# Kernel optimization log

Measured on AMD Instinct MI355X. Metric: run time of the kernel, lower is better.

The kernel has to match this reference:

```python
import jax, jax.numpy as jnp
import numpy as np

N = 20000      # nodes
E = 640000     # edges (avg degree 32)
F_IN = 128     # node_features
H = 128        # hidden_channels
OUT = 64       # output_features


def setup_inputs() -> dict:
    key = jax.random.key(0)
    ks = jax.random.split(key, 12)
    s = 0.05
    return {
        "x": jax.random.normal(ks[0], (N, F_IN), jnp.float32),
        "edge_index": jax.random.randint(ks[1], (2, E), 0, N, dtype=jnp.int64),
        "W1": jax.random.normal(ks[2], (F_IN, H), jnp.float32) * s,
        "b1": jnp.zeros((H,), jnp.float32),
        "W2": jax.random.normal(ks[3], (H, H), jnp.float32) * s,
        "b2": jnp.zeros((H,), jnp.float32),
        "W_ih": jax.random.normal(ks[4], (4 * H, H), jnp.float32) * s,
        "W_hh": jax.random.normal(ks[5], (4 * H, H), jnp.float32) * s,
        "b_ih": jnp.zeros((4 * H,), jnp.float32),
        "b_hh": jnp.zeros((4 * H,), jnp.float32),
        "W_lin": jax.random.normal(ks[6], (OUT, H), jnp.float32) * s,
        "b_lin": jnp.zeros((OUT,), jnp.float32),
    }


def gcn_conv(x, edge_index, W, b):
    # PyG GCNConv: add self-loops, symmetric normalization D^-1/2 A D^-1/2
    n = x.shape[0]
    loop = jnp.arange(n, dtype=edge_index.dtype)
    src = jnp.concatenate([edge_index[0], loop])
    dst = jnp.concatenate([edge_index[1], loop])
    deg = jax.ops.segment_sum(jnp.ones(src.shape[0], x.dtype), dst, num_segments=n)
    dinv = jnp.where(deg > 0, jax.lax.rsqrt(deg), 0.0)
    norm = dinv[src] * dinv[dst]                 # [E+N]
    xw = x @ W                                   # [N, H] transform before aggregate
    msg = xw[src] * norm[:, None]                # gather + scale
    out = jax.ops.segment_sum(msg, dst, num_segments=n)  # scatter-add
    return out + b


def lstm_seq(xs, W_ih, W_hh, b_ih, b_hh):
    # single-layer LSTM over sequence xs: [T, H_in], batch of 1 (squeezed).
    h_dim = W_hh.shape[1]
    h0 = jnp.zeros((h_dim,), xs.dtype)

    def step(carry, xt):
        h, c = carry
        g = xt @ W_ih.T + b_ih + h @ W_hh.T + b_hh
        i, f, gg, o = jnp.split(g, 4)
        i = jax.nn.sigmoid(i)
        f = jax.nn.sigmoid(f)
        gg = jnp.tanh(gg)
        o = jax.nn.sigmoid(o)
        c = f * c + i * gg
        h = o * jnp.tanh(c)
        return (h, c), h

    _, hs = jax.lax.scan(step, (h0, h0), xs)
    return hs  # [T, H]


def reference(x, edge_index, W1, b1, W2, b2, W_ih, W_hh, b_ih, b_hh, W_lin, b_lin):
    h = jax.nn.relu(gcn_conv(x, edge_index, W1, b1))
    # dropout(p=0.2) is identity in eval mode
    h = jax.nn.relu(gcn_conv(h, edge_index, W2, b2))
    hs = lstm_seq(h, W_ih, W_hh, b_ih, b_hh)     # nodes treated as one sequence
    return hs @ W_lin.T + b_lin                  # [N, OUT]
```

## Files before the change

kernel.cpp:

```cpp
#include <hip/hip_runtime.h>
#include <cstdint>

#define NF 128
#define G4 512

typedef float v2f __attribute__((ext_vector_type(2)));

__device__ __forceinline__ float frcp(float x) { return __builtin_amdgcn_rcpf(x); }
__device__ __forceinline__ float ftanh(float x) {
  float e = __expf(2.f * x);
  return 1.f - 2.f * frcp(e + 1.f);
}

__device__ __forceinline__ float dpp_xor1(float x) {
  int r = __builtin_amdgcn_update_dpp(0, __float_as_int(x), 0xB1, 0xF, 0xF, true);
  return __int_as_float(r);
}
__device__ __forceinline__ float dpp_xor2(float x) {
  int r = __builtin_amdgcn_update_dpp(0, __float_as_int(x), 0x4E, 0xF, 0xF, true);
  return __int_as_float(r);
}


__global__ void k_fill(float* p, float v, int n) {
  int i = blockIdx.x * blockDim.x + threadIdx.x;
  if (i < n) p[i] = v;
}

__global__ void k_detect_i64(const int* e, int npairs, int* flag) {
  int f = 1;
  for (int i = 1; i < 2 * npairs; i += 2)
    if (e[i] != 0) { f = 0; break; }
  *flag = f;
}

__device__ __forceinline__ int eidx(const void* edges, int i64, size_t pos) {
  if (i64) return (int)((const long long*)edges)[pos];
  return ((const int*)edges)[pos];
}

__global__ void k_count(const void* __restrict__ edges, const int* __restrict__ flag,
                        float* __restrict__ deg, int E) {
  int e = blockIdx.x * blockDim.x + threadIdx.x;
  if (e < E) {
    int d = eidx(edges, *flag, (size_t)E + e);
    unsafeAtomicAdd(&deg[d], 1.0f);
  }
}

__global__ void k_rsqrt(float* p, int n) {
  int i = blockIdx.x * blockDim.x + threadIdx.x;
  if (i < n) p[i] = rsqrtf(p[i]);
}

__global__ void k_t128(const float* __restrict__ in, float* __restrict__ out) {
  int n = blockIdx.x, k = threadIdx.x;
  out[n * 128 + k] = in[k * 128 + n];
}

__global__ void k_add(const float* a, const float* b, float* o, int n) {
  int i = blockIdx.x * blockDim.x + threadIdx.x;
  if (i < n) o[i] = a[i] + b[i];
}

__global__ void k_wprep(const float* __restrict__ W, float* __restrict__ wp) {
  int t = blockIdx.x;
  int j = threadIdx.x;
  int u = t >> 2, p = t & 3;
  int g = j >> 5, k = j & 31;
  wp[(size_t)t * 128 + j] = W[(size_t)(g * 128 + u) * 128 + 32 * p + k];
}

__global__ __launch_bounds__(256)
void gemm_bt(const float* __restrict__ A, const float* __restrict__ B,
             const float* __restrict__ bias, float* __restrict__ C,
             int M, int N, int K) {
  __shared__ float As[32][68];
  __shared__ float Bs[32][68];
  const int bm = blockIdx.x * 64;
  const int bn = blockIdx.y * 64;
  const int tid = threadIdx.x;
  const int tm = (tid & 15) << 2;
  const int tn = (tid >> 4) << 2;
  float acc[4][4] = {};

  for (int k0 = 0; k0 < K; k0 += 32) {
#pragma unroll
    for (int l = 0; l < 2; ++l) {
      int idx = tid + l * 256;
      int row = idx >> 3;
      int k4 = (idx & 7) << 2;
      int ar = bm + row; ar = ar < M ? ar : M - 1;
      float4 av = *(const float4*)(A + (size_t)ar * K + k0 + k4);
      As[k4 + 0][row] = av.x; As[k4 + 1][row] = av.y;
      As[k4 + 2][row] = av.z; As[k4 + 3][row] = av.w;
      int br = bn + row; br = br < N ? br : N - 1;
      float4 bv = *(const float4*)(B + (size_t)br * K + k0 + k4);
      Bs[k4 + 0][row] = bv.x; Bs[k4 + 1][row] = bv.y;
      Bs[k4 + 2][row] = bv.z; Bs[k4 + 3][row] = bv.w;
    }
    __syncthreads();
#pragma unroll
    for (int kk = 0; kk < 32; ++kk) {
      float4 a = *(const float4*)&As[kk][tm];
      float4 b = *(const float4*)&Bs[kk][tn];
      float av[4] = {a.x, a.y, a.z, a.w};
      float bv[4] = {b.x, b.y, b.z, b.w};
#pragma unroll
      for (int i = 0; i < 4; ++i)
#pragma unroll
        for (int jj = 0; jj < 4; ++jj)
          acc[i][jj] = __builtin_fmaf(av[i], bv[jj], acc[i][jj]);
    }
    __syncthreads();
  }

  float4 bv4;
  if (bias) bv4 = *(const float4*)(bias + bn + tn);
  else bv4 = make_float4(0.f, 0.f, 0.f, 0.f);
#pragma unroll
  for (int i = 0; i < 4; ++i) {
    int row = bm + tm + i;
    if (row < M) {
      float4 v;
      v.x = acc[i][0] + bv4.x;
      v.y = acc[i][1] + bv4.y;
      v.z = acc[i][2] + bv4.z;
      v.w = acc[i][3] + bv4.w;
      *(float4*)(C + (size_t)row * N + bn + tn) = v;
    }
  }
}

__global__ __launch_bounds__(256)
void k_aggregate(const float* __restrict__ xw, const void* __restrict__ edges,
                 const int* __restrict__ flag, const float* __restrict__ dinv,
                 float* __restrict__ out, int E) {
  int e = blockIdx.x * 8 + (threadIdx.x >> 5);
  if (e >= E) return;
  int i64 = *flag;
  int s = eidx(edges, i64, e);
  int d = eidx(edges, i64, (size_t)E + e);
  float nrm = dinv[s] * dinv[d];
  int f4 = threadIdx.x & 31;
  float4 v = ((const float4*)xw)[(size_t)s * 32 + f4];
  float* op = out + (size_t)d * 128 + f4 * 4;
  unsafeAtomicAdd(op + 0, v.x * nrm);
  unsafeAtomicAdd(op + 1, v.y * nrm);
  unsafeAtomicAdd(op + 2, v.z * nrm);
  unsafeAtomicAdd(op + 3, v.w * nrm);
}

__global__ void k_finish(float* __restrict__ h, const float* __restrict__ xw,
                         const float* __restrict__ dinv, const float* __restrict__ b,
                         int N) {
  int i4 = blockIdx.x * blockDim.x + threadIdx.x;
  if (i4 >= N * 32) return;
  int n = i4 >> 5;
  int f4 = (i4 & 31) << 2;
  float di = dinv[n];
  float s = di * di;
  float4 ag = ((const float4*)h)[i4];
  float4 xv = ((const float4*)xw)[i4];
  float4 bv = *(const float4*)(b + f4);
  float4 r;
  r.x = fmaxf(__builtin_fmaf(xv.x, s, ag.x) + bv.x, 0.f);
  r.y = fmaxf(__builtin_fmaf(xv.y, s, ag.y) + bv.y, 0.f);
  r.z = fmaxf(__builtin_fmaf(xv.z, s, ag.z) + bv.z, 0.f);
  r.w = fmaxf(__builtin_fmaf(xv.w, s, ag.w) + bv.w, 0.f);
  ((float4*)h)[i4] = r;
}

__global__ __launch_bounds__(512)
__attribute__((amdgpu_waves_per_eu(2, 2)))
void k_lstm(const float* __restrict__ g_in, const float* __restrict__ wp,
            float* __restrict__ hs, int T) {
  const int t = threadIdx.x;
  const int q = t >> 2;
  const int pos = t & 3;
  const int row = pos * 128 + q;

  __shared__ __align__(16) float hbuf[2][144];
  __shared__ float lds_cap[20736];

  if (t == 0) {
    volatile float* vp = lds_cap;
    vp[0] = 0.f;
  }

  {
    const float* wr = wp + (size_t)t * 128;
    asm volatile(
      "global_load_dwordx4 v[128:131], %0, off\n\t"
      "global_load_dwordx4 v[132:135], %0, off offset:16\n\t"
      "global_load_dwordx4 v[136:139], %0, off offset:32\n\t"
      "global_load_dwordx4 v[140:143], %0, off offset:48\n\t"
      "global_load_dwordx4 v[144:147], %0, off offset:64\n\t"
      "global_load_dwordx4 v[148:151], %0, off offset:80\n\t"
      "global_load_dwordx4 v[152:155], %0, off offset:96\n\t"
      "global_load_dwordx4 v[156:159], %0, off offset:112\n\t"
      "global_load_dwordx4 v[160:163], %0, off offset:128\n\t"
      "global_load_dwordx4 v[164:167], %0, off offset:144\n\t"
      "global_load_dwordx4 v[168:171], %0, off offset:160\n\t"
      "global_load_dwordx4 v[172:175], %0, off offset:176\n\t"
      "global_load_dwordx4 v[176:179], %0, off offset:192\n\t"
      "global_load_dwordx4 v[180:183], %0, off offset:208\n\t"
      "global_load_dwordx4 v[184:187], %0, off offset:224\n\t"
      "global_load_dwordx4 v[188:191], %0, off offset:240\n\t"
      "global_load_dwordx4 v[192:195], %0, off offset:256\n\t"
      "global_load_dwordx4 v[196:199], %0, off offset:272\n\t"
      "global_load_dwordx4 v[200:203], %0, off offset:288\n\t"
      "global_load_dwordx4 v[204:207], %0, off offset:304\n\t"
      "global_load_dwordx4 v[208:211], %0, off offset:320\n\t"
      "global_load_dwordx4 v[212:215], %0, off offset:336\n\t"
      "global_load_dwordx4 v[216:219], %0, off offset:352\n\t"
      "global_load_dwordx4 v[220:223], %0, off offset:368\n\t"
      "global_load_dwordx4 v[224:227], %0, off offset:384\n\t"
      "global_load_dwordx4 v[228:231], %0, off offset:400\n\t"
      "global_load_dwordx4 v[232:235], %0, off offset:416\n\t"
      "global_load_dwordx4 v[236:239], %0, off offset:432\n\t"
      "global_load_dwordx4 v[240:243], %0, off offset:448\n\t"
      "global_load_dwordx4 v[244:247], %0, off offset:464\n\t"
      "global_load_dwordx4 v[248:251], %0, off offset:480\n\t"
      "global_load_dwordx4 v[252:255], %0, off offset:496\n\t"
      "s_waitcnt vmcnt(0)"
      :: "v"(wr)
      : "v128","v129","v130","v131","v132","v133","v134","v135",
        "v136","v137","v138","v139","v140","v141","v142","v143",
        "v144","v145","v146","v147","v148","v149","v150","v151",
        "v152","v153","v154","v155","v156","v157","v158","v159",
        "v160","v161","v162","v163","v164","v165","v166","v167",
        "v168","v169","v170","v171","v172","v173","v174","v175",
        "v176","v177","v178","v179","v180","v181","v182","v183",
        "v184","v185","v186","v187","v188","v189","v190","v191",
        "v192","v193","v194","v195","v196","v197","v198","v199",
        "v200","v201","v202","v203","v204","v205","v206","v207",
        "v208","v209","v210","v211","v212","v213","v214","v215",
        "v216","v217","v218","v219","v220","v221","v222","v223",
        "v224","v225","v226","v227","v228","v229","v230","v231",
        "v232","v233","v234","v235","v236","v237","v238","v239",
        "v240","v241","v242","v243","v244","v245","v246","v247",
        "v248","v249","v250","v251","v252","v253","v254","v255");
  }

  if (t < 144) { hbuf[0][t] = 0.f; hbuf[1][t] = 0.f; }
  float c = 0.f;
  float gn = g_in[row];

  const uint32_t adr0 = (uint32_t)(uintptr_t)&hbuf[0][36 * pos];
  const uint32_t adr1 = (uint32_t)(uintptr_t)&hbuf[1][36 * pos];

  __syncthreads();

  int pb = 0;
  const bool isg = (pos == 2);
  const bool sw1 = (pos & 1);
  const bool sw2 = (pos & 2) != 0;

  for (int step = 0; step < T; ++step) {
    float gcur = gn;
    size_t nb = (size_t)(step + 1 < T ? step + 1 : step) * G4;
    gn = g_in[nb + row];

    uint32_t adr = pb ? adr1 : adr0;
    v2f a0, a1, a2, a3;
    asm volatile(
      "ds_read_b128 v[96:99], %4\n\t"
      "ds_read_b128 v[100:103], %4 offset:16\n\t"
      "ds_read_b128 v[104:107], %4 offset:32\n\t"
      "ds_read_b128 v[108:111], %4 offset:48\n\t"
      "ds_read_b128 v[112:115], %4 offset:64\n\t"
      "ds_read_b128 v[116:119], %4 offset:80\n\t"
      "ds_read_b128 v[120:123], %4 offset:96\n\t"
      "ds_read_b128 v[124:127], %4 offset:112\n\t"
      "s_waitcnt lgkmcnt(0)\n\t"
      "v_pk_mul_f32 %0, v[128:129], v[96:97]\n\t"
      "v_pk_mul_f32 %1, v[160:161], v[96:97]\n\t"
      "v_pk_mul_f32 %2, v[192:193], v[96:97]\n\t"
      "v_pk_mul_f32 %3, v[224:225], v[96:97]\n\t"
      "v_pk_fma_f32 %0, v[130:131], v[98:99], %0\n\t"
      "v_pk_fma_f32 %1, v[162:163], v[98:99], %1\n\t"
      "v_pk_fma_f32 %2, v[194:195], v[98:99], %2\n\t"
      "v_pk_fma_f32 %3, v[226:227], v[98:99], %3\n\t"
      "v_pk_fma_f32 %0, v[132:133], v[100:101], %0\n\t"
      "v_pk_fma_f32 %1, v[164:165], v[100:101], %1\n\t"
      "v_pk_fma_f32 %2, v[196:197], v[100:101], %2\n\t"
      "v_pk_fma_f32 %3, v[228:229], v[100:101], %3\n\t"
      "v_pk_fma_f32 %0, v[134:135], v[102:103], %0\n\t"
      "v_pk_fma_f32 %1, v[166:167], v[102:103], %1\n\t"
      "v_pk_fma_f32 %2, v[198:199], v[102:103], %2\n\t"
      "v_pk_fma_f32 %3, v[230:231], v[102:103], %3\n\t"
      "v_pk_fma_f32 %0, v[136:137], v[104:105], %0\n\t"
      "v_pk_fma_f32 %1, v[168:169], v[104:105], %1\n\t"
      "v_pk_fma_f32 %2, v[200:201], v[104:105], %2\n\t"
      "v_pk_fma_f32 %3, v[232:233], v[104:105], %3\n\t"
      "v_pk_fma_f32 %0, v[138:139], v[106:107], %0\n\t"
      "v_pk_fma_f32 %1, v[170:171], v[106:107], %1\n\t"
      "v_pk_fma_f32 %2, v[202:203], v[106:107], %2\n\t"
      "v_pk_fma_f32 %3, v[234:235], v[106:107], %3\n\t"
      "v_pk_fma_f32 %0, v[140:141], v[108:109], %0\n\t"
      "v_pk_fma_f32 %1, v[172:173], v[108:109], %1\n\t"
      "v_pk_fma_f32 %2, v[204:205], v[108:109], %2\n\t"
      "v_pk_fma_f32 %3, v[236:237], v[108:109], %3\n\t"
      "v_pk_fma_f32 %0, v[142:143], v[110:111], %0\n\t"
      "v_pk_fma_f32 %1, v[174:175], v[110:111], %1\n\t"
      "v_pk_fma_f32 %2, v[206:207], v[110:111], %2\n\t"
      "v_pk_fma_f32 %3, v[238:239], v[110:111], %3\n\t"
      "v_pk_fma_f32 %0, v[144:145], v[112:113], %0\n\t"
      "v_pk_fma_f32 %1, v[176:177], v[112:113], %1\n\t"
      "v_pk_fma_f32 %2, v[208:209], v[112:113], %2\n\t"
      "v_pk_fma_f32 %3, v[240:241], v[112:113], %3\n\t"
      "v_pk_fma_f32 %0, v[146:147], v[114:115], %0\n\t"
      "v_pk_fma_f32 %1, v[178:179], v[114:115], %1\n\t"
      "v_pk_fma_f32 %2, v[210:211], v[114:115], %2\n\t"
      "v_pk_fma_f32 %3, v[242:243], v[114:115], %3\n\t"
      "v_pk_fma_f32 %0, v[148:149], v[116:117], %0\n\t"
      "v_pk_fma_f32 %1, v[180:181], v[116:117], %1\n\t"
      "v_pk_fma_f32 %2, v[212:213], v[116:117], %2\n\t"
      "v_pk_fma_f32 %3, v[244:245], v[116:117], %3\n\t"
      "v_pk_fma_f32 %0, v[150:151], v[118:119], %0\n\t"
      "v_pk_fma_f32 %1, v[182:183], v[118:119], %1\n\t"
      "v_pk_fma_f32 %2, v[214:215], v[118:119], %2\n\t"
      "v_pk_fma_f32 %3, v[246:247], v[118:119], %3\n\t"
      "v_pk_fma_f32 %0, v[152:153], v[120:121], %0\n\t"
      "v_pk_fma_f32 %1, v[184:185], v[120:121], %1\n\t"
      "v_pk_fma_f32 %2, v[216:217], v[120:121], %2\n\t"
      "v_pk_fma_f32 %3, v[248:249], v[120:121], %3\n\t"
      "v_pk_fma_f32 %0, v[154:155], v[122:123], %0\n\t"
      "v_pk_fma_f32 %1, v[186:187], v[122:123], %1\n\t"
      "v_pk_fma_f32 %2, v[218:219], v[122:123], %2\n\t"
      "v_pk_fma_f32 %3, v[250:251], v[122:123], %3\n\t"
      "v_pk_fma_f32 %0, v[156:157], v[124:125], %0\n\t"
      "v_pk_fma_f32 %1, v[188:189], v[124:125], %1\n\t"
      "v_pk_fma_f32 %2, v[220:221], v[124:125], %2\n\t"
      "v_pk_fma_f32 %3, v[252:253], v[124:125], %3\n\t"
      "v_pk_fma_f32 %0, v[158:159], v[126:127], %0\n\t"
      "v_pk_fma_f32 %1, v[190:191], v[126:127], %1\n\t"
      "v_pk_fma_f32 %2, v[222:223], v[126:127], %2\n\t"
      "v_pk_fma_f32 %3, v[254:255], v[126:127], %3"
      : "=&v"(a0), "=&v"(a1), "=&v"(a2), "=&v"(a3)
      : "v"(adr)
      : "memory",
        "v96","v97","v98","v99","v100","v101","v102","v103",
        "v104","v105","v106","v107","v108","v109","v110","v111",
        "v112","v113","v114","v115","v116","v117","v118","v119",
        "v120","v121","v122","v123","v124","v125","v126","v127");

    float s0 = a0.x + a0.y;
    float s1 = a1.x + a1.y;
    float s2 = a2.x + a2.y;
    float s3 = a3.x + a3.y;

    float send_lo = sw1 ? s0 : s1;
    float send_hi = sw1 ? s2 : s3;
    float keep_lo = sw1 ? s1 : s0;
    float keep_hi = sw1 ? s3 : s2;
    float r_lo = keep_lo + dpp_xor1(send_lo);
    float r_hi = keep_hi + dpp_xor1(send_hi);
    float send2 = sw2 ? r_lo : r_hi;
    float keep2 = sw2 ? r_hi : r_lo;
    float x = keep2 + dpp_xor2(send2) + gcur;

    float xs = isg ? 2.f * x : x;
    float e = __expf(-xs);
    float r = frcp(1.f + e);
    float a = isg ? 2.f * r - 1.f : r;

    float b = dpp_xor1(a);
    float c2 = dpp_xor2(a);
    float d2 = dpp_xor2(b);
    float p0 = sw1 ? b : a;
    float p1 = sw1 ? a : b;
    float p2 = sw1 ? d2 : c2;
    float p3 = sw1 ? c2 : d2;
    float i_ = sw2 ? p2 : p0;
    float f_ = sw2 ? p3 : p1;
    float g_ = sw2 ? p0 : p2;
    float o_ = sw2 ? p1 : p3;

    c = __builtin_fmaf(f_, c, i_ * g_);
    float h = o_ * ftanh(c);

    pb ^= 1;
    if (pos == 0) {
      hbuf[pb][q + ((q >> 5) << 2)] = h;
      hs[(size_t)step * NF + q] = h;
    }
    __syncthreads();
  }
}


extern "C" void kernel_launch(void* const* d_in, const int* in_sizes, int n_in,
                              void* d_out, int out_size, void* d_ws, size_t ws_size,
                              hipStream_t stream) {
  const float* x     = (const float*)d_in[0];
  const void* edges  = d_in[1];
  const float* W1    = (const float*)d_in[2];
  const float* b1    = (const float*)d_in[3];
  const float* W2    = (const float*)d_in[4];
  const float* b2    = (const float*)d_in[5];
  const float* W_ih  = (const float*)d_in[6];
  const float* W_hh  = (const float*)d_in[7];
  const float* b_ih  = (const float*)d_in[8];
  const float* b_hh  = (const float*)d_in[9];
  const float* W_lin = (const float*)d_in[10];
  const float* b_lin = (const float*)d_in[11];
  float* out = (float*)d_out;

  const int N = in_sizes[0] / NF;
  const int E = in_sizes[1] / 2;
  const int OUTF = 64;

  char* base = (char*)d_ws;
  size_t off = 0;
  auto alloc = [&](size_t b) {
    char* p = base + off;
    off += (b + 255) & ~(size_t)255;
    return p;
  };
  float* dinv = (float*)alloc((size_t)N * 4);
  float* W1T  = (float*)alloc(128 * 128 * 4);
  float* W2T  = (float*)alloc(128 * 128 * 4);
  float* wp   = (float*)alloc(512 * 128 * 4);
  float* bsum = (float*)alloc(512 * 4);
  int*   flag = (int*)alloc(256);
  float* bufA = (float*)alloc((size_t)N * NF * 4);
  float* bufB = (float*)alloc((size_t)N * NF * 4);
  float* bufC = (float*)alloc((size_t)N * NF * 4);
  float* g_in = (float*)alloc((size_t)N * (size_t)G4 * 4);
  if (off > ws_size) return;

  k_fill<<<(N + 255) / 256, 256, 0, stream>>>(dinv, 1.0f, N);
  k_detect_i64<<<1, 1, 0, stream>>>((const int*)edges, 1024, flag);
  k_count<<<(E + 255) / 256, 256, 0, stream>>>(edges, flag, dinv, E);
  k_rsqrt<<<(N + 255) / 256, 256, 0, stream>>>(dinv, N);
  k_t128<<<128, 128, 0, stream>>>(W1, W1T);
  k_t128<<<128, 128, 0, stream>>>(W2, W2T);
  k_wprep<<<512, 128, 0, stream>>>(W_hh, wp);
  k_add<<<2, 256, 0, stream>>>(b_ih, b_hh, bsum, 512);

  const int mg = (N + 63) / 64;

  gemm_bt<<<dim3(mg, 2), 256, 0, stream>>>(x, W1T, nullptr, bufA, N, NF, NF);
  hipMemsetAsync(bufB, 0, (size_t)N * NF * 4, stream);
  k_aggregate<<<(E + 7) / 8, 256, 0, stream>>>(bufA, edges, flag, dinv, bufB, E);
  k_finish<<<(N * 32 + 255) / 256, 256, 0, stream>>>(bufB, bufA, dinv, b1, N);

  gemm_bt<<<dim3(mg, 2), 256, 0, stream>>>(bufB, W2T, nullptr, bufA, N, NF, NF);
  hipMemsetAsync(bufC, 0, (size_t)N * NF * 4, stream);
  k_aggregate<<<(E + 7) / 8, 256, 0, stream>>>(bufA, edges, flag, dinv, bufC, E);
  k_finish<<<(N * 32 + 255) / 256, 256, 0, stream>>>(bufC, bufA, dinv, b2, N);

  gemm_bt<<<dim3(mg, 8), 256, 0, stream>>>(bufC, W_ih, bsum, g_in, N, G4, NF);

  k_lstm<<<1, 512, 0, stream>>>(g_in, wp, bufB, N);

  gemm_bt<<<dim3(mg, 1), 256, 0, stream>>>(bufB, W_lin, b_lin, out, N, OUTF, NF);
}
```

Baseline: 13.89 ms.

## Split LSTM recurrent dot product across 8 lanes with swizzled weight layout

The serial LSTM step now splits each gate's 128-wide hidden-state dot product over 8 lanes of 16 elements, instead of 4 lanes of 32. That halves the LDS reads of h per thread, with 8 packed accumulators per thread. The weight prep is re-laid out with an XOR swizzle so each lane's 16-wide slice lines up with a conflict-free hbuf layout (stride 20). LDS waits are staged so FMAs can start as each 16-byte read lands. The cost is a deeper cross-lane reduction that adds a ds_swizzle xor-4 step, which itself goes through the LDS path on the critical path of every step.

```diff
diff --git a/kernel.cpp b/kernel.cpp
--- a/kernel.cpp
+++ b/kernel.cpp
@@ -19,6 +19,9 @@
 __device__ __forceinline__ float dpp_xor2(float x) {
   int r = __builtin_amdgcn_update_dpp(0, __float_as_int(x), 0x4E, 0xF, 0xF, true);
   return __int_as_float(r);
+}
+__device__ __forceinline__ float swz_xor4(float x) {
+  return __int_as_float(__builtin_amdgcn_ds_swizzle(__float_as_int(x), 0x101F));
 }
 
 
@@ -65,10 +68,16 @@
 
 __global__ void k_wprep(const float* __restrict__ W, float* __restrict__ wp) {
   int t = blockIdx.x;
-  int j = threadIdx.x;
-  int u = t >> 2, p = t & 3;
-  int g = j >> 5, k = j & 31;
-  wp[(size_t)t * 128 + j] = W[(size_t)(g * 128 + u) * 128 + 32 * p + k];
+  int m = threadIdx.x;
+  int j = t & 7;
+  int g8 = t >> 3;
+  int blk = m >> 4;
+  int k = m & 15;
+  int rr = j ^ blk;
+  int gate = rr & 3, du = rr >> 2;
+  int unit = 2 * g8 + du;
+  int col = 16 * j + k;
+  wp[(size_t)t * 128 + m] = W[(size_t)(gate * 128 + unit) * 128 + col];
 }
 
 __global__ __launch_bounds__(256)
@@ -176,11 +185,14 @@
 void k_lstm(const float* __restrict__ g_in, const float* __restrict__ wp,
             float* __restrict__ hs, int T) {
   const int t = threadIdx.x;
-  const int q = t >> 2;
+  const int j = t & 7;
+  const int g8 = t >> 3;
   const int pos = t & 3;
-  const int row = pos * 128 + q;
-
-  __shared__ __align__(16) float hbuf[2][144];
+  const int du = (t >> 2) & 1;
+  const int unit = 2 * g8 + du;
+  const int row = pos * 128 + unit;
+
+  __shared__ __align__(16) float hbuf[2][160];
   __shared__ float lds_cap[20736];
 
   if (t == 0) {
@@ -243,12 +255,12 @@
         "v248","v249","v250","v251","v252","v253","v254","v255");
   }
 
-  if (t < 144) { hbuf[0][t] = 0.f; hbuf[1][t] = 0.f; }
+  if (t < 160) { hbuf[0][t] = 0.f; hbuf[1][t] = 0.f; }
   float c = 0.f;
   float gn = g_in[row];
 
-  const uint32_t adr0 = (uint32_t)(uintptr_t)&hbuf[0][36 * pos];
-  const uint32_t adr1 = (uint32_t)(uintptr_t)&hbuf[1][36 * pos];
+  const uint32_t adr0 = (uint32_t)(uintptr_t)&hbuf[0][20 * j];
+  const uint32_t adr1 = (uint32_t)(uintptr_t)&hbuf[1][20 * j];
 
   __syncthreads();
 
@@ -263,103 +275,99 @@
     gn = g_in[nb + row];
 
     uint32_t adr = pb ? adr1 : adr0;
-    v2f a0, a1, a2, a3;
+    v2f a0, a1, a2, a3, a4, a5, a6, a7;
     asm volatile(
-      "ds_read_b128 v[96:99], %4\n\t"
-      "ds_read_b128 v[100:103], %4 offset:16\n\t"
-      "ds_read_b128 v[104:107], %4 offset:32\n\t"
-      "ds_read_b128 v[108:111], %4 offset:48\n\t"
-      "ds_read_b128 v[112:115], %4 offset:64\n\t"
-      "ds_read_b128 v[116:119], %4 offset:80\n\t"
-      "ds_read_b128 v[120:123], %4 offset:96\n\t"
-      "ds_read_b128 v[124:127], %4 offset:112\n\t"
+      "ds_read_b128 v[96:99], %8\n\t"
+      "ds_read_b128 v[100:103], %8 offset:16\n\t"
+      "ds_read_b128 v[104:107], %8 offset:32\n\t"
+      "ds_read_b128 v[108:111], %8 offset:48\n\t"
+      "s_waitcnt lgkmcnt(3)\n\t"
+      "v_pk_mul_f32 %0, v[128:129], v[96:97]\n\t"
+      "v_pk_mul_f32 %1, v[144:145], v[96:97]\n\t"
+      "v_pk_mul_f32 %2, v[160:161], v[96:97]\n\t"
+      "v_pk_mul_f32 %3, v[176:177], v[96:97]\n\t"
+      "v_pk_mul_f32 %4, v[192:193], v[96:97]\n\t"
+      "v_pk_mul_f32 %5, v[208:209], v[96:97]\n\t"
+      "v_pk_mul_f32 %6, v[224:225], v[96:97]\n\t"
+      "v_pk_mul_f32 %7, v[240:241], v[96:97]\n\t"
+      "v_pk_fma_f32 %0, v[130:131], v[98:99], %0\n\t"
+      "v_pk_fma_f32 %1, v[146:147], v[98:99], %1\n\t"
+      "v_pk_fma_f32 %2, v[162:163], v[98:99], %2\n\t"
+      "v_pk_fma_f32 %3, v[178:179], v[98:99], %3\n\t"
+      "v_pk_fma_f32 %4, v[194:195], v[98:99], %4\n\t"
+      "v_pk_fma_f32 %5, v[210:211], v[98:99], %5\n\t"
+      "v_pk_fma_f32 %6, v[226:227], v[98:99], %6\n\t"
+      "v_pk_fma_f32 %7, v[242:243], v[98:99], %7\n\t"
+      "s_waitcnt lgkmcnt(2)\n\t"
+      "v_pk_fma_f32 %0, v[132:133], v[100:101], %0\n\t"
+      "v_pk_fma_f32 %1, v[148:149], v[100:101], %1\n\t"
+      "v_pk_fma_f32 %2, v[164:165], v[100:101], %2\n\t"
+      "v_pk_fma_f32 %3, v[180:181], v[100:101], %3\n\t"
+      "v_pk_fma_f32 %4, v[196:197], v[100:101], %4\n\t"
+      "v_pk_fma_f32 %5, v[212:213], v[100:101], %5\n\t"
+      "v_pk_fma_f32 %6, v[228:229], v[100:101], %6\n\t"
+      "v_pk_fma_f32 %7, v[244:245], v[100:101], %7\n\t"
+      "v_pk_fma_f32 %0, v[134:135], v[102:103], %0\n\t"
+      "v_pk_fma_f32 %1, v[150:151], v[102:103], %1\n\t"
+      "v_pk_fma_f32 %2, v[166:167], v[102:103], %2\n\t"
+      "v_pk_fma_f32 %3, v[182:183], v[102:103], %3\n\t"
+      "v_pk_fma_f32 %4, v[198:199], v[102:103], %4\n\t"
+      "v_pk_fma_f32 %5, v[214:215], v[102:103], %5\n\t"
+      "v_pk_fma_f32 %6, v[230:231], v[102:103], %6\n\t"
+      "v_pk_fma_f32 %7, v[246:247], v[102:103], %7\n\t"
+      "s_waitcnt lgkmcnt(1)\n\t"
+      "v_pk_fma_f32 %0, v[136:137], v[104:105], %0\n\t"
+      "v_pk_fma_f32 %1, v[152:153], v[104:105], %1\n\t"
+      "v_pk_fma_f32 %2, v[168:169], v[104:105], %2\n\t"
+      "v_pk_fma_f32 %3, v[184:185], v[104:105], %3\n\t"
+      "v_pk_fma_f32 %4, v[200:201], v[104:105], %4\n\t"
+      "v_pk_fma_f32 %5, v[216:217], v[104:105], %5\n\t"
+      "v_pk_fma_f32 %6, v[232:233], v[104:105], %6\n\t"
+      "v_pk_fma_f32 %7, v[248:249], v[104:105], %7\n\t"
+      "v_pk_fma_f32 %0, v[138:139], v[106:107], %0\n\t"
+      "v_pk_fma_f32 %1, v[154:155], v[106:107], %1\n\t"
+      "v_pk_fma_f32 %2, v[170:171], v[106:107], %2\n\t"
+      "v_pk_fma_f32 %3, v[186:187], v[106:107], %3\n\t"
+      "v_pk_fma_f32 %4, v[202:203], v[106:107], %4\n\t"
+      "v_pk_fma_f32 %5, v[218:219], v[106:107], %5\n\t"
+      "v_pk_fma_f32 %6, v[234:235], v[106:107], %6\n\t"
+      "v_pk_fma_f32 %7, v[250:251], v[106:107], %7\n\t"
       "s_waitcnt lgkmcnt(0)\n\t"
-      "v_pk_mul_f32 %0, v[128:129], v[96:97]\n\t"
-      "v_pk_mul_f32 %1, v[160:161], v[96:97]\n\t"
-      "v_pk_mul_f32 %2, v[192:193], v[96:97]\n\t"
-      "v_pk_mul_f32 %3, v[224:225], v[96:97]\n\t"
-      "v_pk_fma_f32 %0, v[130:131], v[98:99], %0\n\t"
-      "v_pk_fma_f32 %1, v[162:163], v[98:99], %1\n\t"
-      "v_pk_fma_f32 %2, v[194:195], v[98:99], %2\n\t"
-      "v_pk_fma_f32 %3, v[226:227], v[98:99], %3\n\t"
-      "v_pk_fma_f32 %0, v[132:133], v[100:101], %0\n\t"
-      "v_pk_fma_f32 %1, v[164:165], v[100:101], %1\n\t"
-      "v_pk_fma_f32 %2, v[196:197], v[100:101], %2\n\t"
-      "v_pk_fma_f32 %3, v[228:229], v[100:101], %3\n\t"
-      "v_pk_fma_f32 %0, v[134:135], v[102:103], %0\n\t"
-      "v_pk_fma_f32 %1, v[166:167], v[102:103], %1\n\t"
-      "v_pk_fma_f32 %2, v[198:199], v[102:103], %2\n\t"
-      "v_pk_fma_f32 %3, v[230:231], v[102:103], %3\n\t"
-      "v_pk_fma_f32 %0, v[136:137], v[104:105], %0\n\t"
-      "v_pk_fma_f32 %1, v[168:169], v[104:105], %1\n\t"
-      "v_pk_fma_f32 %2, v[200:201], v[104:105], %2\n\t"
-      "v_pk_fma_f32 %3, v[232:233], v[104:105], %3\n\t"
-      "v_pk_fma_f32 %0, v[138:139], v[106:107], %0\n\t"
-      "v_pk_fma_f32 %1, v[170:171], v[106:107], %1\n\t"
-      "v_pk_fma_f32 %2, v[202:203], v[106:107], %2\n\t"
-      "v_pk_fma_f32 %3, v[234:235], v[106:107], %3\n\t"
       "v_pk_fma_f32 %0, v[140:141], v[108:109], %0\n\t"
-      "v_pk_fma_f32 %1, v[172:173], v[108:109], %1\n\t"
-      "v_pk_fma_f32 %2, v[204:205], v[108:109], %2\n\t"
-      "v_pk_fma_f32 %3, v[236:237], v[108:109], %3\n\t"
+      "v_pk_fma_f32 %1, v[156:157], v[108:109], %1\n\t"
+      "v_pk_fma_f32 %2, v[172:173], v[108:109], %2\n\t"
+      "v_pk_fma_f32 %3, v[188:189], v[108:109], %3\n\t"
+      "v_pk_fma_f32 %4, v[204:205], v[108:109], %4\n\t"
+      "v_pk_fma_f32 %5, v[220:221], v[108:109], %5\n\t"
+      "v_pk_fma_f32 %6, v[236:237], v[108:109], %6\n\t"
+      "v_pk_fma_f32 %7, v[252:253], v[108:109], %7\n\t"
       "v_pk_fma_f32 %0, v[142:143], v[110:111], %0\n\t"
-      "v_pk_fma_f32 %1, v[174:175], v[110:111], %1\n\t"
-      "v_pk_fma_f32 %2, v[206:207], v[110:111], %2\n\t"
-      "v_pk_fma_f32 %3, v[238:239], v[110:111], %3\n\t"
-      "v_pk_fma_f32 %0, v[144:145], v[112:113], %0\n\t"
-      "v_pk_fma_f32 %1, v[176:177], v[112:113], %1\n\t"
-      "v_pk_fma_f32 %2, v[208:209], v[112:113], %2\n\t"
-      "v_pk_fma_f32 %3, v[240:241], v[112:113], %3\n\t"
-      "v_pk_fma_f32 %0, v[146:147], v[114:115], %0\n\t"
-      "v_pk_fma_f32 %1, v[178:179], v[114:115], %1\n\t"
-      "v_pk_fma_f32 %2, v[210:211], v[114:115], %2\n\t"
-      "v_pk_fma_f32 %3, v[242:243], v[114:115], %3\n\t"
-      "v_pk_fma_f32 %0, v[148:149], v[116:117], %0\n\t"
-      "v_pk_fma_f32 %1, v[180:181], v[116:117], %1\n\t"
-      "v_pk_fma_f32 %2, v[212:213], v[116:117], %2\n\t"
-      "v_pk_fma_f32 %3, v[244:245], v[116:117], %3\n\t"
-      "v_pk_fma_f32 %0, v[150:151], v[118:119], %0\n\t"
-      "v_pk_fma_f32 %1, v[182:183], v[118:119], %1\n\t"
-      "v_pk_fma_f32 %2, v[214:215], v[118:119], %2\n\t"
-      "v_pk_fma_f32 %3, v[246:247], v[118:119], %3\n\t"
-      "v_pk_fma_f32 %0, v[152:153], v[120:121], %0\n\t"
-      "v_pk_fma_f32 %1, v[184:185], v[120:121], %1\n\t"
-      "v_pk_fma_f32 %2, v[216:217], v[120:121], %2\n\t"
-      "v_pk_fma_f32 %3, v[248:249], v[120:121], %3\n\t"
-      "v_pk_fma_f32 %0, v[154:155], v[122:123], %0\n\t"
-      "v_pk_fma_f32 %1, v[186:187], v[122:123], %1\n\t"
-      "v_pk_fma_f32 %2, v[218:219], v[122:123], %2\n\t"
-      "v_pk_fma_f32 %3, v[250:251], v[122:123], %3\n\t"
-      "v_pk_fma_f32 %0, v[156:157], v[124:125], %0\n\t"
-      "v_pk_fma_f32 %1, v[188:189], v[124:125], %1\n\t"
-      "v_pk_fma_f32 %2, v[220:221], v[124:125], %2\n\t"
-      "v_pk_fma_f32 %3, v[252:253], v[124:125], %3\n\t"
-      "v_pk_fma_f32 %0, v[158:159], v[126:127], %0\n\t"
-      "v_pk_fma_f32 %1, v[190:191], v[126:127], %1\n\t"
-      "v_pk_fma_f32 %2, v[222:223], v[126:127], %2\n\t"
-      "v_pk_fma_f32 %3, v[254:255], v[126:127], %3"
-      : "=&v"(a0), "=&v"(a1), "=&v"(a2), "=&v"(a3)
+      "v_pk_fma_f32 %1, v[158:159], v[110:111], %1\n\t"
+      "v_pk_fma_f32 %2, v[174:175], v[110:111], %2\n\t"
+      "v_pk_fma_f32 %3, v[190:191], v[110:111], %3\n\t"
+      "v_pk_fma_f32 %4, v[206:207], v[110:111], %4\n\t"
+      "v_pk_fma_f32 %5, v[222:223], v[110:111], %5\n\t"
+      "v_pk_fma_f32 %6, v[238:239], v[110:111], %6\n\t"
+      "v_pk_fma_f32 %7, v[254:255], v[110:111], %7"
+      : "=&v"(a0), "=&v"(a1), "=&v"(a2), "=&v"(a3),
+        "=&v"(a4), "=&v"(a5), "=&v"(a6), "=&v"(a7)
       : "v"(adr)
       : "memory",
         "v96","v97","v98","v99","v100","v101","v102","v103",
-        "v104","v105","v106","v107","v108","v109","v110","v111",
-        "v112","v113","v114","v115","v116","v117","v118","v119",
-        "v120","v121","v122","v123","v124","v125","v126","v127");
-
-    float s0 = a0.x + a0.y;
-    float s1 = a1.x + a1.y;
-    float s2 = a2.x + a2.y;
-    float s3 = a3.x + a3.y;
-
-    float send_lo = sw1 ? s0 : s1;
-    float send_hi = sw1 ? s2 : s3;
-    float keep_lo = sw1 ? s1 : s0;
-    float keep_hi = sw1 ? s3 : s2;
-    float r_lo = keep_lo + dpp_xor1(send_lo);
-    float r_hi = keep_hi + dpp_xor1(send_hi);
-    float send2 = sw2 ? r_lo : r_hi;
-    float keep2 = sw2 ? r_hi : r_lo;
-    float x = keep2 + dpp_xor2(send2) + gcur;
+        "v104","v105","v106","v107","v108","v109","v110","v111");
+
+    float s0 = a0.x + a0.y, s1 = a1.x + a1.y;
+    float s2 = a2.x + a2.y, s3 = a3.x + a3.y;
+    float s4 = a4.x + a4.y, s5 = a5.x + a5.y;
+    float s6 = a6.x + a6.y, s7 = a7.x + a7.y;
+
+    float r0 = s0 + dpp_xor1(s1);
+    float r2 = s2 + dpp_xor1(s3);
+    float r4 = s4 + dpp_xor1(s5);
+    float r6 = s6 + dpp_xor1(s7);
+    float q0 = r0 + dpp_xor2(r2);
+    float q4 = r4 + dpp_xor2(r6);
+    float x = q0 + swz_xor4(q4) + gcur;
 
     float xs = isg ? 2.f * x : x;
     float e = __expf(-xs);
@@ -383,8 +391,8 @@
 
     pb ^= 1;
     if (pos == 0) {
-      hbuf[pb][q + ((q >> 5) << 2)] = h;
-      hs[(size_t)step * NF + q] = h;
+      hbuf[pb][20 * (unit >> 4) + (unit & 15)] = h;
+      hs[(size_t)step * NF + unit] = h;
     }
     __syncthreads();
   }
```

Result: faster. 13.61 ms (-2.1%).
